# Performance work log

Hardware: AMD Instinct MI355X
Metric: run time of the kernel (lower is better)

The kernel has to match this reference:

```python
import jax, jax.numpy as jnp
import numpy as np


def setup_inputs() -> dict:
    key = jax.random.key(0)
    ks = jax.random.split(key, 5)
    B, H, W, C = 16, 64, 64, 256
    sd = lambda fan_in: 1.0 / np.sqrt(fan_in)
    return {
        "x": jax.random.normal(ks[0], (B, H, W, C), dtype=jnp.float32),
        "Wf": jax.random.normal(ks[1], (C, C // 8), dtype=jnp.float32) * sd(C),
        "bf": jnp.zeros((C // 8,), dtype=jnp.float32),
        "Wg": jax.random.normal(ks[2], (C, C // 8), dtype=jnp.float32) * sd(C),
        "bg": jnp.zeros((C // 8,), dtype=jnp.float32),
        "Wh": jax.random.normal(ks[3], (C, C // 2), dtype=jnp.float32) * sd(C),
        "bh": jnp.zeros((C // 2,), dtype=jnp.float32),
        "Wo": jax.random.normal(ks[4], (C // 2, C), dtype=jnp.float32) * sd(C // 2),
        "bo": jnp.zeros((C,), dtype=jnp.float32),
    }


def reference(x, Wf, bf, Wg, bg, Wh, bh, Wo, bo):
    B, H, W, C = x.shape
    hw = H * W
    # 1x1 convs == per-pixel channel GEMMs
    f = (jnp.einsum('bhwc,cd->bhwd', x, Wf) + bf).reshape(B, hw, -1)  # keys   [B,hw,C/8]
    g = (jnp.einsum('bhwc,cd->bhwd', x, Wg) + bg).reshape(B, hw, -1)  # queries[B,hw,C/8]
    h = (jnp.einsum('bhwc,cd->bhwd', x, Wh) + bh).reshape(B, hw, -1)  # values [B,hw,C/2]
    # full non-causal spatial attention: s = g @ f^T, softmax over keys, @ h
    s = jnp.einsum('bqd,bkd->bqk', g, f)          # [B,hw,hw]
    beta = jax.nn.softmax(s, axis=-1)
    o = jnp.einsum('bqk,bkd->bqd', beta, h)       # [B,hw,C/2]
    o = o.reshape(B, H, W, C // 2)
    o = jnp.einsum('bhwd,dc->bhwc', o, Wo) + bo   # output 1x1 conv to C
    return x + o
```

## Files before the change

### kernel.cpp

```cpp
#include <hip/hip_runtime.h>
#include <hip/hip_bf16.h>
#include <stdint.h>

typedef __attribute__((ext_vector_type(8))) short short8;
typedef __attribute__((ext_vector_type(4))) float floatx4;
typedef __attribute__((ext_vector_type(16))) float floatx16;
typedef __attribute__((ext_vector_type(4))) int int4v;
typedef __attribute__((ext_vector_type(4))) unsigned int uint4v;

#define MFMA16(a, b, c) __builtin_amdgcn_mfma_f32_16x16x32_bf16(a, b, c, 0, 0, 0)
#define MFMA32(a, b, c) __builtin_amdgcn_mfma_f32_32x32x16_bf16(a, b, c, 0, 0, 0)

static constexpr int kHW = 4096;
static constexpr int kC  = 256;
static constexpr int kD  = 32;
static constexpr int kDV = 128;

__device__ __forceinline__ short f2bf(float f) {
  union { float f; uint32_t u; } v; v.f = f;
  uint32_t r = (v.u + 0x7FFFu + ((v.u >> 16) & 1u)) >> 16;
  return (short)(uint16_t)r;
}
__device__ __forceinline__ float bf2f(short s) {
  union { uint32_t u; float f; } v; v.u = ((uint32_t)(uint16_t)s) << 16;
  return v.f;
}
__device__ __forceinline__ void split_bf(float f, short& hi, short& lo) {
  hi = f2bf(f);
  lo = f2bf(f - bf2f(hi));
}
__device__ __forceinline__ uint32_t pk2(float a, float b) {
  return (uint32_t)(uint16_t)f2bf(a) | ((uint32_t)(uint16_t)f2bf(b) << 16);
}
__device__ __forceinline__ short8 mkfrag(uint32_t a, uint32_t b, uint32_t c, uint32_t d) {
  uint4v t = {a, b, c, d};
  return __builtin_bit_cast(short8, t);
}

__global__ __launch_bounds__(256) void prep_kernel(
    const float* __restrict__ Wf, const float* __restrict__ Wg,
    const float* __restrict__ Wh, const float* __restrict__ Wo,
    short* __restrict__ Wt_h, short* __restrict__ Wt_l,
    short* __restrict__ Wot_h, short* __restrict__ Wot_l) {
  const int i = blockIdx.x * 256 + threadIdx.x;
  const int total1 = 192 * 256;
  if (i < total1) {
    int c = i >> 8, k = i & 255;
    float wv;
    if (c < 32)       wv = Wf[(size_t)k * 32 + c];
    else if (c < 64)  wv = Wg[(size_t)k * 32 + (c - 32)];
    else              wv = Wh[(size_t)k * 128 + (c - 64)];
    short h, l; split_bf(wv, h, l);
    Wt_h[i] = h; Wt_l[i] = l;
  } else {
    int j = i - total1;
    int c = j >> 7, k = j & 127;
    short h, l; split_bf(Wo[(size_t)k * 256 + c], h, l);
    Wot_h[j] = h; Wot_l[j] = l;
  }
}

__global__ __launch_bounds__(256, 3) void fgh_kernel(
    const float* __restrict__ x,
    const float* __restrict__ bfv, const float* __restrict__ bgv,
    const float* __restrict__ bhv,
    const short* __restrict__ Wt_h, const short* __restrict__ Wt_l,
    short* __restrict__ f_h, short* __restrict__ f_l,
    short* __restrict__ g_h, short* __restrict__ g_l,
    short* __restrict__ hT) {
  __shared__ short ht2[128][136];

  const int tid  = threadIdx.x;
  const int lane = tid & 63;
  const int w    = tid >> 6;
  const int cl   = lane & 15;
  const int row4 = lane >> 4;
  const int px0  = blockIdx.x * 128;

  floatx4 acc[2][12];
#pragma unroll
  for (int mt = 0; mt < 2; ++mt)
#pragma unroll
    for (int i = 0; i < 12; ++i) acc[mt][i] = (floatx4){0.f, 0.f, 0.f, 0.f};

#pragma unroll
  for (int kp = 0; kp < 8; ++kp) {
    short8 xh[2], xl[2];
#pragma unroll
    for (int mt = 0; mt < 2; ++mt) {
      const float* xr = x + (size_t)(px0 + w * 32 + mt * 16 + cl) * kC + kp * 32 + row4 * 8;
      float4 v0 = *reinterpret_cast<const float4*>(xr);
      float4 v1 = *reinterpret_cast<const float4*>(xr + 4);
      float vv[8] = {v0.x, v0.y, v0.z, v0.w, v1.x, v1.y, v1.z, v1.w};
#pragma unroll
      for (int e = 0; e < 8; ++e) {
        short h, l; split_bf(vv[e], h, l);
        xh[mt][e] = h; xl[mt][e] = l;
      }
    }
#pragma unroll
    for (int ct = 0; ct < 12; ++ct) {
      const size_t woff = (size_t)(ct * 16 + cl) * 256 + kp * 32 + row4 * 8;
      short8 bh_ = *reinterpret_cast<const short8*>(Wt_h + woff);
      short8 bl_ = *reinterpret_cast<const short8*>(Wt_l + woff);
#pragma unroll
      for (int mt = 0; mt < 2; ++mt) {
        acc[mt][ct] = MFMA16(xh[mt], bh_, acc[mt][ct]);
        acc[mt][ct] = MFMA16(xh[mt], bl_, acc[mt][ct]);
        acc[mt][ct] = MFMA16(xl[mt], bh_, acc[mt][ct]);
      }
    }
  }

#pragma unroll
  for (int mt = 0; mt < 2; ++mt)
#pragma unroll
    for (int ct = 0; ct < 4; ++ct) {
      int c = ct * 16 + cl;
      float bias = (c < 32) ? bfv[c] : bgv[c - 32];
      const int cc = (c < 32) ? c : (c - 32);
      short* dh = (c < 32) ? f_h : g_h;
      short* dl = (c < 32) ? f_l : g_l;
#pragma unroll
      for (int j = 0; j < 4; ++j) {
        int pix = px0 + w * 32 + mt * 16 + row4 * 4 + j;
        short h, l; split_bf(acc[mt][ct][j] + bias, h, l);
        dh[(size_t)pix * kD + cc] = h;
        dl[(size_t)pix * kD + cc] = l;
      }
    }

#pragma unroll
  for (int mt = 0; mt < 2; ++mt)
#pragma unroll
    for (int ct = 4; ct < 12; ++ct) {
      int dv = (ct - 4) * 16 + cl;
      float bias = bhv[dv];
#pragma unroll
      for (int j = 0; j < 4; ++j)
        ht2[dv][w * 32 + mt * 16 + row4 * 4 + j] = f2bf(acc[mt][ct][j] + bias);
    }
  __syncthreads();
  const int b   = px0 >> 12;
  const int pb0 = px0 & 4095;
#pragma unroll
  for (int it = 0; it < 8; ++it) {
    int c = tid + it * 256;
    int dv = c >> 4, p8 = c & 15;
    int4v v = *reinterpret_cast<const int4v*>(&ht2[dv][p8 * 8]);
    *reinterpret_cast<int4v*>(hT + ((size_t)(b * kDV + dv)) * kHW + pb0 + p8 * 8) = v;
  }
}

__global__ __launch_bounds__(256, 3) void attn_kernel(
    const short* __restrict__ fkh, const short* __restrict__ fkl,
    const short* __restrict__ gqh, const short* __restrict__ gql,
    const short* __restrict__ hT,
    short* __restrict__ og) {
  __shared__ __align__(16) char smem[34816];
  char* Vb = smem;

  const int tid  = threadIdx.x;
  const int lane = tid & 63;
  const int w    = tid >> 6;
  const int cl   = lane & 31;
  const int hi   = lane >> 5;
  const int bb   = blockIdx.x >> 5;
  const int q0   = (blockIdx.x & 31) * 128;
  const int qw   = q0 + w * 32;

  const size_t qbase = ((size_t)bb * kHW + qw + cl) * kD + hi * 8;
  const short8 qh0 = *reinterpret_cast<const short8*>(gqh + qbase);
  const short8 qh1 = *reinterpret_cast<const short8*>(gqh + qbase + 16);
  const short8 ql0 = *reinterpret_cast<const short8*>(gql + qbase);
  const short8 ql1 = *reinterpret_cast<const short8*>(gql + qbase + 16);

  const floatx16 z16 = {0.f,0.f,0.f,0.f,0.f,0.f,0.f,0.f,0.f,0.f,0.f,0.f,0.f,0.f,0.f,0.f};
  floatx16 acc[4];
#pragma unroll
  for (int i = 0; i < 4; ++i) acc[i] = z16;
  float m = -1e30f, ls = 0.f;

  for (int kb0 = 0; kb0 < 32; ++kb0) {
    __syncthreads();
#pragma unroll
    for (int it = 0; it < 8; ++it) {
      int c = tid + it * 256;
      int dv = c >> 4, k16 = c & 15;
      uint4v v = *reinterpret_cast<const uint4v*>(
          hT + ((size_t)(bb * kDV + dv)) * kHW + kb0 * 128 + k16 * 8);
      *reinterpret_cast<uint4v*>(Vb + dv * 256 + ((k16 * 16) ^ ((dv & 15) << 4))) = v;
    }
    __syncthreads();

#pragma unroll
    for (int t = 0; t < 4; ++t) {
      const int kk = kb0 * 128 + t * 32;
      const size_t kbse = ((size_t)bb * kHW + kk + cl) * kD + hi * 8;
      short8 kh0 = *reinterpret_cast<const short8*>(fkh + kbse);
      short8 kh1 = *reinterpret_cast<const short8*>(fkh + kbse + 16);
      short8 kl0 = *reinterpret_cast<const short8*>(fkl + kbse);
      short8 kl1 = *reinterpret_cast<const short8*>(fkl + kbse + 16);

      floatx16 sA = MFMA32(kh0, qh0, z16);
      sA = MFMA32(kh1, qh1, sA);
      sA = MFMA32(kl0, qh0, sA);
      floatx16 sB = MFMA32(kl1, qh1, z16);
      sB = MFMA32(kh0, ql0, sB);
      sB = MFMA32(kh1, ql1, sB);

      float pr[16];
      float tm = -1e30f;
#pragma unroll
      for (int r = 0; r < 16; ++r) {
        float sv = sA[r] + sB[r];
        pr[r] = sv;
        tm = fmaxf(tm, sv);
      }
      tm = fmaxf(tm, __shfl_xor(tm, 32));

      if (__any(tm > m + 8.0f)) {
        float mn = fmaxf(m, tm);
        float sc = __expf(m - mn);
        ls *= sc;
#pragma unroll
        for (int ct = 0; ct < 4; ++ct)
#pragma unroll
          for (int r = 0; r < 16; ++r) acc[ct][r] *= sc;
        m = mn;
      }

      float sum = 0.f;
#pragma unroll
      for (int r = 0; r < 16; ++r) {
        pr[r] = __expf(pr[r] - m);
        sum += pr[r];
      }
      ls += sum;

      uint32_t pk[8], X[8];
#pragma unroll
      for (int i = 0; i < 8; ++i) pk[i] = pk2(pr[2 * i], pr[2 * i + 1]);
#pragma unroll
      for (int i = 0; i < 8; ++i) X[i] = (uint32_t)__shfl_xor((int)pk[i], 32);
      short8 pf0 = mkfrag(hi ? X[2] : pk[0], hi ? X[3] : pk[1],
                          hi ? pk[2] : X[0], hi ? pk[3] : X[1]);
      short8 pf1 = mkfrag(hi ? X[6] : pk[4], hi ? X[7] : pk[5],
                          hi ? pk[6] : X[4], hi ? pk[7] : X[5]);

      __builtin_amdgcn_s_setprio(1);
#pragma unroll
      for (int ct = 0; ct < 4; ++ct) {
        int dv = ct * 32 + cl;
        short8 va = *reinterpret_cast<const short8*>(
            Vb + dv * 256 + (((t * 2 + 0) * 32 + hi * 16) ^ ((dv & 15) << 4)));
        acc[ct] = MFMA32(va, pf0, acc[ct]);
      }
#pragma unroll
      for (int ct = 0; ct < 4; ++ct) {
        int dv = ct * 32 + cl;
        short8 va = *reinterpret_cast<const short8*>(
            Vb + dv * 256 + (((t * 2 + 1) * 32 + hi * 16) ^ ((dv & 15) << 4)));
        acc[ct] = MFMA32(va, pf1, acc[ct]);
      }
      __builtin_amdgcn_s_setprio(0);
    }
  }

  ls += __shfl_xor(ls, 32);
  const float inv = 1.0f / ls;

  __syncthreads();
  short* ot = reinterpret_cast<short*>(smem) + w * 32 * 136;
#pragma unroll
  for (int ct = 0; ct < 4; ++ct)
#pragma unroll
    for (int r = 0; r < 16; ++r) {
      int dv = ct * 32 + (r & 3) + 8 * (r >> 2) + 4 * hi;
      ot[cl * 136 + dv] = f2bf(acc[ct][r] * inv);
    }
  __syncthreads();
#pragma unroll
  for (int it = 0; it < 8; ++it) {
    int q2 = it * 4 + (lane >> 4);
    int ck = lane & 15;
    int4v v = *reinterpret_cast<const int4v*>(ot + q2 * 136 + ck * 8);
    *reinterpret_cast<int4v*>(og + ((size_t)bb * kHW + qw + q2) * kDV + ck * 8) = v;
  }
}

__global__ __launch_bounds__(256, 4) void outproj_kernel(
    const short* __restrict__ o,
    const short* __restrict__ Wot_h, const short* __restrict__ Wot_l,
    const float* __restrict__ bo,
    const float* __restrict__ x,
    float* __restrict__ out) {
  const int tid  = threadIdx.x;
  const int lane = tid & 63;
  const int w    = tid >> 6;
  const int cl   = lane & 15;
  const int row4 = lane >> 4;
  const int px0  = blockIdx.x * 64;

  floatx4 acc[16];
#pragma unroll
  for (int i = 0; i < 16; ++i) acc[i] = (floatx4){0.f, 0.f, 0.f, 0.f};

#pragma unroll
  for (int kp = 0; kp < 4; ++kp) {
    short8 a = *reinterpret_cast<const short8*>(
        o + (size_t)(px0 + w * 16 + cl) * kDV + kp * 32 + row4 * 8);
#pragma unroll
    for (int ct = 0; ct < 16; ++ct) {
      const size_t woff = (size_t)(ct * 16 + cl) * 128 + kp * 32 + row4 * 8;
      short8 bh_ = *reinterpret_cast<const short8*>(Wot_h + woff);
      short8 bl_ = *reinterpret_cast<const short8*>(Wot_l + woff);
      acc[ct] = MFMA16(a, bh_, acc[ct]);
      acc[ct] = MFMA16(a, bl_, acc[ct]);
    }
  }

#pragma unroll
  for (int ct = 0; ct < 16; ++ct) {
    int c = ct * 16 + cl;
    float bias = bo[c];
#pragma unroll
    for (int j = 0; j < 4; ++j) {
      size_t idx = (size_t)(px0 + w * 16 + row4 * 4 + j) * kC + c;
      out[idx] = x[idx] + acc[ct][j] + bias;
    }
  }
}

extern "C" void kernel_launch(void* const* d_in, const int* in_sizes, int n_in,
                              void* d_out, int out_size, void* d_ws, size_t ws_size,
                              hipStream_t stream) {
  const float* x  = (const float*)d_in[0];
  const float* Wf = (const float*)d_in[1];
  const float* bf = (const float*)d_in[2];
  const float* Wg = (const float*)d_in[3];
  const float* bg = (const float*)d_in[4];
  const float* Wh = (const float*)d_in[5];
  const float* bh = (const float*)d_in[6];
  const float* Wo = (const float*)d_in[7];
  const float* bo = (const float*)d_in[8];
  float* out = (float*)d_out;

  char* ws = (char*)d_ws;
  const size_t MB = 1024 * 1024;
  short* f_h = (short*)(ws);
  short* f_l = (short*)(ws + 4  * MB);
  short* g_h = (short*)(ws + 8  * MB);
  short* g_l = (short*)(ws + 12 * MB);
  short* hT  = (short*)(ws + 16 * MB);
  short* o   = (short*)(ws + 32 * MB);
  short* Wt_h  = (short*)(ws + 48 * MB);
  short* Wt_l  = (short*)(ws + 48 * MB + 98304);
  short* Wot_h = (short*)(ws + 48 * MB + 196608);
  short* Wot_l = (short*)(ws + 48 * MB + 262144);

  prep_kernel<<<320, 256, 0, stream>>>(Wf, Wg, Wh, Wo, Wt_h, Wt_l, Wot_h, Wot_l);
  fgh_kernel<<<512, 256, 0, stream>>>(x, bf, bg, bh, Wt_h, Wt_l,
                                      f_h, f_l, g_h, g_l, hT);
  attn_kernel<<<512, 256, 0, stream>>>(f_h, f_l, g_h, g_l, hT, o);
  outproj_kernel<<<1024, 256, 0, stream>>>(o, Wot_h, Wot_l, bo, x, out);
}
```

Baseline: 424.1 us.

## Double-buffer V tiles in attention, shrink fgh tiles, use permlane32 swap and cheaper bf16 pack

The attention kernel now double-buffers the V tile in 64KB of LDS, prefetching the next block into registers while computing the current one. This removes one of the two barriers per key block and hides the global load latency. P fragments are built with permlane32_swap instead of eight shuffles, and bf16 packing uses a byte-permute with round-half-up rather than round-to-nearest-even. The two score accumulators are merged into one chain and the max is computed as a tree. The fgh kernel processes 64 pixels per block with 1024 blocks and a higher occupancy target, while the attention kernel drops to an occupancy target of 2, which risks lower latency hiding.

```diff
diff --git a/kernel.cpp b/kernel.cpp
--- a/kernel.cpp
+++ b/kernel.cpp
@@ -7,6 +7,7 @@
 typedef __attribute__((ext_vector_type(16))) float floatx16;
 typedef __attribute__((ext_vector_type(4))) int int4v;
 typedef __attribute__((ext_vector_type(4))) unsigned int uint4v;
+typedef __attribute__((ext_vector_type(2))) unsigned int uint2v;
 
 #define MFMA16(a, b, c) __builtin_amdgcn_mfma_f32_16x16x32_bf16(a, b, c, 0, 0, 0)
 #define MFMA32(a, b, c) __builtin_amdgcn_mfma_f32_32x32x16_bf16(a, b, c, 0, 0, 0)
@@ -29,8 +30,11 @@
   hi = f2bf(f);
   lo = f2bf(f - bf2f(hi));
 }
-__device__ __forceinline__ uint32_t pk2(float a, float b) {
-  return (uint32_t)(uint16_t)f2bf(a) | ((uint32_t)(uint16_t)f2bf(b) << 16);
+__device__ __forceinline__ uint32_t fbits(float f) {
+  union { float f; uint32_t u; } v; v.f = f; return v.u;
+}
+__device__ __forceinline__ uint32_t pk2(float e, float o) {
+  return __builtin_amdgcn_perm(fbits(o) + 0x8000u, fbits(e) + 0x8000u, 0x07060302u);
 }
 __device__ __forceinline__ short8 mkfrag(uint32_t a, uint32_t b, uint32_t c, uint32_t d) {
   uint4v t = {a, b, c, d};
@@ -60,7 +64,7 @@
   }
 }
 
-__global__ __launch_bounds__(256, 3) void fgh_kernel(
+__global__ __launch_bounds__(256, 4) void fgh_kernel(
     const float* __restrict__ x,
     const float* __restrict__ bfv, const float* __restrict__ bgv,
     const float* __restrict__ bhv,
@@ -68,97 +72,84 @@
     short* __restrict__ f_h, short* __restrict__ f_l,
     short* __restrict__ g_h, short* __restrict__ g_l,
     short* __restrict__ hT) {
-  __shared__ short ht2[128][136];
+  __shared__ short ht2[128][72];
 
   const int tid  = threadIdx.x;
   const int lane = tid & 63;
   const int w    = tid >> 6;
   const int cl   = lane & 15;
   const int row4 = lane >> 4;
-  const int px0  = blockIdx.x * 128;
-
-  floatx4 acc[2][12];
-#pragma unroll
-  for (int mt = 0; mt < 2; ++mt)
-#pragma unroll
-    for (int i = 0; i < 12; ++i) acc[mt][i] = (floatx4){0.f, 0.f, 0.f, 0.f};
+  const int px0  = blockIdx.x * 64;
+
+  floatx4 acc[12];
+#pragma unroll
+  for (int i = 0; i < 12; ++i) acc[i] = (floatx4){0.f, 0.f, 0.f, 0.f};
 
 #pragma unroll
   for (int kp = 0; kp < 8; ++kp) {
-    short8 xh[2], xl[2];
-#pragma unroll
-    for (int mt = 0; mt < 2; ++mt) {
-      const float* xr = x + (size_t)(px0 + w * 32 + mt * 16 + cl) * kC + kp * 32 + row4 * 8;
-      float4 v0 = *reinterpret_cast<const float4*>(xr);
-      float4 v1 = *reinterpret_cast<const float4*>(xr + 4);
-      float vv[8] = {v0.x, v0.y, v0.z, v0.w, v1.x, v1.y, v1.z, v1.w};
-#pragma unroll
-      for (int e = 0; e < 8; ++e) {
-        short h, l; split_bf(vv[e], h, l);
-        xh[mt][e] = h; xl[mt][e] = l;
-      }
+    const float* xr = x + (size_t)(px0 + w * 16 + cl) * kC + kp * 32 + row4 * 8;
+    float4 v0 = *reinterpret_cast<const float4*>(xr);
+    float4 v1 = *reinterpret_cast<const float4*>(xr + 4);
+    float vv[8] = {v0.x, v0.y, v0.z, v0.w, v1.x, v1.y, v1.z, v1.w};
+    short8 xh, xl;
+#pragma unroll
+    for (int e = 0; e < 8; ++e) {
+      short h, l; split_bf(vv[e], h, l);
+      xh[e] = h; xl[e] = l;
     }
 #pragma unroll
     for (int ct = 0; ct < 12; ++ct) {
       const size_t woff = (size_t)(ct * 16 + cl) * 256 + kp * 32 + row4 * 8;
       short8 bh_ = *reinterpret_cast<const short8*>(Wt_h + woff);
       short8 bl_ = *reinterpret_cast<const short8*>(Wt_l + woff);
-#pragma unroll
-      for (int mt = 0; mt < 2; ++mt) {
-        acc[mt][ct] = MFMA16(xh[mt], bh_, acc[mt][ct]);
-        acc[mt][ct] = MFMA16(xh[mt], bl_, acc[mt][ct]);
-        acc[mt][ct] = MFMA16(xl[mt], bh_, acc[mt][ct]);
-      }
-    }
-  }
-
-#pragma unroll
-  for (int mt = 0; mt < 2; ++mt)
-#pragma unroll
-    for (int ct = 0; ct < 4; ++ct) {
-      int c = ct * 16 + cl;
-      float bias = (c < 32) ? bfv[c] : bgv[c - 32];
-      const int cc = (c < 32) ? c : (c - 32);
-      short* dh = (c < 32) ? f_h : g_h;
-      short* dl = (c < 32) ? f_l : g_l;
-#pragma unroll
-      for (int j = 0; j < 4; ++j) {
-        int pix = px0 + w * 32 + mt * 16 + row4 * 4 + j;
-        short h, l; split_bf(acc[mt][ct][j] + bias, h, l);
-        dh[(size_t)pix * kD + cc] = h;
-        dl[(size_t)pix * kD + cc] = l;
-      }
-    }
-
-#pragma unroll
-  for (int mt = 0; mt < 2; ++mt)
-#pragma unroll
-    for (int ct = 4; ct < 12; ++ct) {
-      int dv = (ct - 4) * 16 + cl;
-      float bias = bhv[dv];
-#pragma unroll
-      for (int j = 0; j < 4; ++j)
-        ht2[dv][w * 32 + mt * 16 + row4 * 4 + j] = f2bf(acc[mt][ct][j] + bias);
-    }
+      acc[ct] = MFMA16(xh, bh_, acc[ct]);
+      acc[ct] = MFMA16(xh, bl_, acc[ct]);
+      acc[ct] = MFMA16(xl, bh_, acc[ct]);
+    }
+  }
+
+#pragma unroll
+  for (int ct = 0; ct < 4; ++ct) {
+    int c = ct * 16 + cl;
+    float bias = (c < 32) ? bfv[c] : bgv[c - 32];
+    const int cc = (c < 32) ? c : (c - 32);
+    short* dh = (c < 32) ? f_h : g_h;
+    short* dl = (c < 32) ? f_l : g_l;
+#pragma unroll
+    for (int j = 0; j < 4; ++j) {
+      int pix = px0 + w * 16 + row4 * 4 + j;
+      short h, l; split_bf(acc[ct][j] + bias, h, l);
+      dh[(size_t)pix * kD + cc] = h;
+      dl[(size_t)pix * kD + cc] = l;
+    }
+  }
+
+#pragma unroll
+  for (int ct = 4; ct < 12; ++ct) {
+    int dv = (ct - 4) * 16 + cl;
+    float bias = bhv[dv];
+#pragma unroll
+    for (int j = 0; j < 4; ++j)
+      ht2[dv][w * 16 + row4 * 4 + j] = f2bf(acc[ct][j] + bias);
+  }
   __syncthreads();
   const int b   = px0 >> 12;
   const int pb0 = px0 & 4095;
 #pragma unroll
-  for (int it = 0; it < 8; ++it) {
+  for (int it = 0; it < 4; ++it) {
     int c = tid + it * 256;
-    int dv = c >> 4, p8 = c & 15;
+    int dv = c >> 3, p8 = c & 7;
     int4v v = *reinterpret_cast<const int4v*>(&ht2[dv][p8 * 8]);
     *reinterpret_cast<int4v*>(hT + ((size_t)(b * kDV + dv)) * kHW + pb0 + p8 * 8) = v;
   }
 }
 
-__global__ __launch_bounds__(256, 3) void attn_kernel(
+__global__ __launch_bounds__(256, 2) void attn_kernel(
     const short* __restrict__ fkh, const short* __restrict__ fkl,
     const short* __restrict__ gqh, const short* __restrict__ gql,
     const short* __restrict__ hT,
     short* __restrict__ og) {
-  __shared__ __align__(16) char smem[34816];
-  char* Vb = smem;
+  __shared__ __align__(16) char smem[65536];
 
   const int tid  = threadIdx.x;
   const int lane = tid & 63;
@@ -169,6 +160,10 @@
   const int q0   = (blockIdx.x & 31) * 128;
   const int qw   = q0 + w * 32;
 
+  const int  sdv  = tid >> 4;
+  const int  sk16 = tid & 15;
+  const short* hTb = hT + (size_t)bb * kDV * kHW;
+
   const size_t qbase = ((size_t)bb * kHW + qw + cl) * kD + hi * 8;
   const short8 qh0 = *reinterpret_cast<const short8*>(gqh + qbase);
   const short8 qh1 = *reinterpret_cast<const short8*>(gqh + qbase + 16);
@@ -181,42 +176,64 @@
   for (int i = 0; i < 4; ++i) acc[i] = z16;
   float m = -1e30f, ls = 0.f;
 
-  for (int kb0 = 0; kb0 < 32; ++kb0) {
-    __syncthreads();
-#pragma unroll
-    for (int it = 0; it < 8; ++it) {
-      int c = tid + it * 256;
-      int dv = c >> 4, k16 = c & 15;
-      uint4v v = *reinterpret_cast<const uint4v*>(
-          hT + ((size_t)(bb * kDV + dv)) * kHW + kb0 * 128 + k16 * 8);
-      *reinterpret_cast<uint4v*>(Vb + dv * 256 + ((k16 * 16) ^ ((dv & 15) << 4))) = v;
-    }
-    __syncthreads();
+  uint4v vr[8];
+#pragma unroll
+  for (int it = 0; it < 8; ++it) {
+    int dv = sdv + it * 16;
+    vr[it] = *reinterpret_cast<const uint4v*>(hTb + (size_t)dv * kHW + 0 * 128 + sk16 * 8);
+  }
+#pragma unroll
+  for (int it = 0; it < 8; ++it) {
+    int dv = sdv + it * 16;
+    *reinterpret_cast<uint4v*>(smem + dv * 256 + ((sk16 * 16) ^ ((dv & 15) << 4))) = vr[it];
+  }
+#pragma unroll
+  for (int it = 0; it < 8; ++it) {
+    int dv = sdv + it * 16;
+    vr[it] = *reinterpret_cast<const uint4v*>(hTb + (size_t)dv * kHW + 1 * 128 + sk16 * 8);
+  }
+  __syncthreads();
+
+  for (int kb = 0; kb < 32; ++kb) {
+    char* Vb = smem + (kb & 1) * 32768;
+    if (kb + 1 < 32) {
+      char* Vn = smem + ((kb + 1) & 1) * 32768;
+#pragma unroll
+      for (int it = 0; it < 8; ++it) {
+        int dv = sdv + it * 16;
+        *reinterpret_cast<uint4v*>(Vn + dv * 256 + ((sk16 * 16) ^ ((dv & 15) << 4))) = vr[it];
+      }
+      if (kb + 2 < 32) {
+#pragma unroll
+        for (int it = 0; it < 8; ++it) {
+          int dv = sdv + it * 16;
+          vr[it] = *reinterpret_cast<const uint4v*>(
+              hTb + (size_t)dv * kHW + (kb + 2) * 128 + sk16 * 8);
+        }
+      }
+    }
 
 #pragma unroll
     for (int t = 0; t < 4; ++t) {
-      const int kk = kb0 * 128 + t * 32;
+      const int kk = kb * 128 + t * 32;
       const size_t kbse = ((size_t)bb * kHW + kk + cl) * kD + hi * 8;
       short8 kh0 = *reinterpret_cast<const short8*>(fkh + kbse);
       short8 kh1 = *reinterpret_cast<const short8*>(fkh + kbse + 16);
       short8 kl0 = *reinterpret_cast<const short8*>(fkl + kbse);
       short8 kl1 = *reinterpret_cast<const short8*>(fkl + kbse + 16);
 
-      floatx16 sA = MFMA32(kh0, qh0, z16);
-      sA = MFMA32(kh1, qh1, sA);
-      sA = MFMA32(kl0, qh0, sA);
-      floatx16 sB = MFMA32(kl1, qh1, z16);
-      sB = MFMA32(kh0, ql0, sB);
-      sB = MFMA32(kh1, ql1, sB);
-
-      float pr[16];
-      float tm = -1e30f;
-#pragma unroll
-      for (int r = 0; r < 16; ++r) {
-        float sv = sA[r] + sB[r];
-        pr[r] = sv;
-        tm = fmaxf(tm, sv);
-      }
+      floatx16 s = MFMA32(kh0, qh0, z16);
+      s = MFMA32(kh1, qh1, s);
+      s = MFMA32(kl0, qh0, s);
+      s = MFMA32(kl1, qh1, s);
+      s = MFMA32(kh0, ql0, s);
+      s = MFMA32(kh1, ql1, s);
+
+      float tm = fmaxf(fmaxf(s[0], s[1]), fmaxf(s[2], s[3]));
+      tm = fmaxf(tm, fmaxf(fmaxf(s[4], s[5]), fmaxf(s[6], s[7])));
+      float tm2 = fmaxf(fmaxf(s[8], s[9]), fmaxf(s[10], s[11]));
+      tm2 = fmaxf(tm2, fmaxf(fmaxf(s[12], s[13]), fmaxf(s[14], s[15])));
+      tm = fmaxf(tm, tm2);
       tm = fmaxf(tm, __shfl_xor(tm, 32));
 
       if (__any(tm > m + 8.0f)) {
@@ -230,23 +247,30 @@
         m = mn;
       }
 
+      float pr[16];
       float sum = 0.f;
 #pragma unroll
       for (int r = 0; r < 16; ++r) {
-        pr[r] = __expf(pr[r] - m);
+        pr[r] = __expf(s[r] - m);
         sum += pr[r];
       }
       ls += sum;
 
-      uint32_t pk[8], X[8];
+      uint32_t pk[8];
 #pragma unroll
       for (int i = 0; i < 8; ++i) pk[i] = pk2(pr[2 * i], pr[2 * i + 1]);
-#pragma unroll
-      for (int i = 0; i < 8; ++i) X[i] = (uint32_t)__shfl_xor((int)pk[i], 32);
-      short8 pf0 = mkfrag(hi ? X[2] : pk[0], hi ? X[3] : pk[1],
-                          hi ? pk[2] : X[0], hi ? pk[3] : X[1]);
-      short8 pf1 = mkfrag(hi ? X[6] : pk[4], hi ? X[7] : pk[5],
-                          hi ? pk[6] : X[4], hi ? pk[7] : X[5]);
+      {
+        uint2v r0 = __builtin_amdgcn_permlane32_swap(pk[0], pk[2], false, false);
+        pk[0] = r0.x; pk[2] = r0.y;
+        uint2v r1 = __builtin_amdgcn_permlane32_swap(pk[1], pk[3], false, false);
+        pk[1] = r1.x; pk[3] = r1.y;
+        uint2v r2 = __builtin_amdgcn_permlane32_swap(pk[4], pk[6], false, false);
+        pk[4] = r2.x; pk[6] = r2.y;
+        uint2v r3 = __builtin_amdgcn_permlane32_swap(pk[5], pk[7], false, false);
+        pk[5] = r3.x; pk[7] = r3.y;
+      }
+      short8 pf0 = mkfrag(pk[0], pk[1], pk[2], pk[3]);
+      short8 pf1 = mkfrag(pk[4], pk[5], pk[6], pk[7]);
 
       __builtin_amdgcn_s_setprio(1);
 #pragma unroll
@@ -265,12 +289,12 @@
       }
       __builtin_amdgcn_s_setprio(0);
     }
+    __syncthreads();
   }
 
   ls += __shfl_xor(ls, 32);
   const float inv = 1.0f / ls;
 
-  __syncthreads();
   short* ot = reinterpret_cast<short*>(smem) + w * 32 * 136;
 #pragma unroll
   for (int ct = 0; ct < 4; ++ct)
@@ -360,8 +384,8 @@
   short* Wot_l = (short*)(ws + 48 * MB + 262144);
 
   prep_kernel<<<320, 256, 0, stream>>>(Wf, Wg, Wh, Wo, Wt_h, Wt_l, Wot_h, Wot_l);
-  fgh_kernel<<<512, 256, 0, stream>>>(x, bf, bg, bh, Wt_h, Wt_l,
-                                      f_h, f_l, g_h, g_l, hT);
+  fgh_kernel<<<1024, 256, 0, stream>>>(x, bf, bg, bh, Wt_h, Wt_l,
+                                       f_h, f_l, g_h, g_l, hT);
   attn_kernel<<<512, 256, 0, stream>>>(f_h, f_l, g_h, g_l, hT, o);
   outproj_kernel<<<1024, 256, 0, stream>>>(o, Wot_h, Wot_l, bo, x, out);
 }
```

Result: slower. 450.2 us (+6.2%).
